# Performance work log

Hardware: AMD Instinct MI355X
Metric: run time of the kernel (lower is better)

Reference implementation:

```python
import jax, jax.numpy as jnp
import numpy as np

N = 100000   # nodes
E = 1600000  # edges
G = 512      # graphs in batch
F_IN = 128
H = 128
F_OUT = 1


def setup_inputs() -> dict:
    key = jax.random.key(0)
    ks = jax.random.split(key, 12)
    x = jax.random.normal(ks[0], (N, F_IN), dtype=jnp.float32)
    src = jax.random.randint(ks[1], (E,), 0, N, dtype=jnp.int32)
    dst = jax.random.randint(ks[2], (E,), 0, N, dtype=jnp.int32)
    node2graph = jnp.sort(jax.random.randint(ks[3], (N,), 0, G, dtype=jnp.int32))
    s_in = 1.0 / np.sqrt(F_IN)
    s_h = 1.0 / np.sqrt(H)
    W0 = jax.random.normal(ks[4], (F_IN, H), dtype=jnp.float32) * s_in
    b0 = jnp.zeros((H,), dtype=jnp.float32)
    W1 = jax.random.normal(ks[5], (H, H), dtype=jnp.float32) * s_h
    b1 = jnp.zeros((H,), dtype=jnp.float32)
    W2 = jax.random.normal(ks[6], (H, H), dtype=jnp.float32) * s_h
    b2 = jnp.zeros((H,), dtype=jnp.float32)
    Wm1 = jax.random.normal(ks[7], (H, H), dtype=jnp.float32) * s_h
    bm1 = jnp.zeros((H,), dtype=jnp.float32)
    Wm2 = jax.random.normal(ks[8], (H, F_OUT), dtype=jnp.float32) * s_h
    bm2 = jnp.zeros((F_OUT,), dtype=jnp.float32)
    return {"x": x, "src": src, "dst": dst, "node2graph": node2graph,
            "W0": W0, "b0": b0, "W1": W1, "b1": b1, "W2": W2, "b2": b2,
            "Wm1": Wm1, "bm1": bm1, "Wm2": Wm2, "bm2": bm2}


def _degree_norms(src, dst):
    ones = jnp.ones((E,), dtype=jnp.float32)
    out_deg = jax.ops.segment_sum(ones, src, num_segments=N)
    in_deg = jax.ops.segment_sum(ones, dst, num_segments=N)
    norm_out = jax.lax.rsqrt(jnp.maximum(out_deg, 1.0))  # [N]
    norm_in = jax.lax.rsqrt(jnp.maximum(in_deg, 1.0))    # [N]
    return norm_out, norm_in


def _graph_conv(x, src, dst, norm_out, norm_in, W, b):
    # DGL GraphConv, norm='both', in_feats <= out_feats path:
    # aggregate normalized src features, then linear + activation.
    xs = x * norm_out[:, None]
    msg = xs[src]                                         # [E, H] gather
    agg = jax.ops.segment_sum(msg, dst, num_segments=N)   # [N, H] scatter-add
    agg = agg * norm_in[:, None]
    return jax.nn.relu(agg @ W + b)


def reference(x, src, dst, node2graph, W0, b0, W1, b1, W2, b2, Wm1, bm1, Wm2, bm2):
    norm_out, norm_in = _degree_norms(src, dst)
    h = _graph_conv(x, src, dst, norm_out, norm_in, W0, b0)
    h = _graph_conv(h, src, dst, norm_out, norm_in, W1, b1)
    h = _graph_conv(h, src, dst, norm_out, norm_in, W2, b2)
    # sum_nodes readout per graph
    g = jax.ops.segment_sum(h, node2graph, num_segments=G)  # [G, H]
    # MLP head: Linear -> ReLU -> Linear
    return jax.nn.relu(g @ Wm1 + bm1) @ Wm2 + bm2           # [G, 1]
```

## Files before the change

### kernel.cpp

```cpp
#include <hip/hip_runtime.h>

#define NN 100000
#define NE 1600000
#define NG 512
#define HD 128

#define NBK 196
#define CHUNK 5120
#define NC 313
#define LH (2 * NBK * NC)

typedef _Float16 half4 __attribute__((ext_vector_type(4)));
typedef _Float16 h8 __attribute__((ext_vector_type(8)));
typedef float f32x4 __attribute__((ext_vector_type(4)));

__global__ __launch_bounds__(256) void k_hist(const int* __restrict__ src,
                                              const int* __restrict__ dst,
                                              int* __restrict__ H) {
    __shared__ int hd[NBK], hs[NBK];
    int c = blockIdx.x;
    for (int i = threadIdx.x; i < NBK; i += 256) { hd[i] = 0; hs[i] = 0; }
    __syncthreads();
    int e0 = c * CHUNK;
    int e1 = e0 + CHUNK; if (e1 > NE) e1 = NE;
    for (int e = e0 + threadIdx.x; e < e1; e += 256) {
        atomicAdd(&hd[dst[e] >> 9], 1);
        atomicAdd(&hs[src[e] >> 9], 1);
    }
    __syncthreads();
    for (int i = threadIdx.x; i < NBK; i += 256) {
        H[i * NC + c] = hd[i];
        H[NBK * NC + i * NC + c] = hs[i];
    }
}

__global__ __launch_bounds__(256) void k_scan1g(int* __restrict__ H,
                                                int* __restrict__ bsum, int L) {
    __shared__ int s[256];
    int i = blockIdx.x * 256 + threadIdx.x;
    int v = (i < L) ? H[i] : 0;
    s[threadIdx.x] = v;
    __syncthreads();
    for (int off = 1; off < 256; off <<= 1) {
        int t = (threadIdx.x >= off) ? s[threadIdx.x - off] : 0;
        __syncthreads();
        s[threadIdx.x] += t;
        __syncthreads();
    }
    if (i < L) H[i] = s[threadIdx.x] - v;
    if (threadIdx.x == 255) bsum[blockIdx.x] = s[255];
}

__global__ __launch_bounds__(512) void k_scan2(int* __restrict__ bsum, int nb) {
    __shared__ int s[512];
    int v = (threadIdx.x < nb) ? bsum[threadIdx.x] : 0;
    s[threadIdx.x] = v;
    __syncthreads();
    for (int off = 1; off < 512; off <<= 1) {
        int t = (threadIdx.x >= off) ? s[threadIdx.x - off] : 0;
        __syncthreads();
        s[threadIdx.x] += t;
        __syncthreads();
    }
    if (threadIdx.x < nb) bsum[threadIdx.x] = s[threadIdx.x] - v;
}

__global__ __launch_bounds__(256) void k_scan3g(int* __restrict__ H,
                                                const int* __restrict__ bsum, int L) {
    int i = blockIdx.x * 256 + threadIdx.x;
    if (i < L) H[i] += bsum[i >> 8];
}

__global__ __launch_bounds__(256) void k_scatter(const int* __restrict__ src,
                                                 const int* __restrict__ dst,
                                                 const int* __restrict__ H,
                                                 int2* __restrict__ dpart,
                                                 int* __restrict__ spart) {
    __shared__ int cd[NBK], cs[NBK];
    int c = blockIdx.x;
    for (int i = threadIdx.x; i < NBK; i += 256) {
        cd[i] = H[i * NC + c];
        cs[i] = H[NBK * NC + i * NC + c] - NE;
    }
    __syncthreads();
    int e0 = c * CHUNK;
    int e1 = e0 + CHUNK; if (e1 > NE) e1 = NE;
    for (int e = e0 + threadIdx.x; e < e1; e += 256) {
        int s = src[e], d = dst[e];
        int pd = atomicAdd(&cd[d >> 9], 1);
        dpart[pd] = make_int2(s, d);
        int ps = atomicAdd(&cs[s >> 9], 1);
        spart[ps] = s;
    }
}

__global__ __launch_bounds__(256) void k_bucket(const int2* __restrict__ dpart,
                                                const int* __restrict__ spart,
                                                const int* __restrict__ H,
                                                int* __restrict__ offs,
                                                int* __restrict__ csr,
                                                float* __restrict__ ni,
                                                float* __restrict__ no) {
    __shared__ int deg[512];
    __shared__ int cur[512];
    __shared__ int tmp[256];
    int b = blockIdx.x;
    bool isDst = (b < NBK);
    int bb = isDst ? b : b - NBK;
    int start, end;
    if (isDst) {
        start = H[bb * NC];
        end = (bb + 1 < NBK) ? H[(bb + 1) * NC] : NE;
    } else {
        start = H[NBK * NC + bb * NC] - NE;
        end = (bb + 1 < NBK) ? H[NBK * NC + (bb + 1) * NC] - NE : NE;
    }
    for (int i = threadIdx.x; i < 512; i += 256) deg[i] = 0;
    __syncthreads();
    if (isDst) {
        for (int i = start + threadIdx.x; i < end; i += 256)
            atomicAdd(&deg[dpart[i].y & 511], 1);
    } else {
        for (int i = start + threadIdx.x; i < end; i += 256)
            atomicAdd(&deg[spart[i] & 511], 1);
    }
    __syncthreads();
    int vb = bb * 512;
    if (!isDst) {
        for (int i = threadIdx.x; i < 512; i += 256) {
            int v = vb + i;
            if (v < NN) no[v] = rsqrtf(fmaxf((float)deg[i], 1.0f));
        }
        return;
    }
    int t = threadIdx.x;
    int a0 = deg[2 * t], a1 = deg[2 * t + 1];
    int pair = a0 + a1;
    tmp[t] = pair;
    __syncthreads();
    for (int off = 1; off < 256; off <<= 1) {
        int v2 = (t >= off) ? tmp[t - off] : 0;
        __syncthreads();
        tmp[t] += v2;
        __syncthreads();
    }
    int ex = tmp[t] - pair;
    cur[2 * t] = start + ex;
    cur[2 * t + 1] = start + ex + a0;
    __syncthreads();
    for (int i = threadIdx.x; i < 512; i += 256) {
        int v = vb + i;
        if (v < NN) {
            offs[v] = cur[i];
            ni[v] = rsqrtf(fmaxf((float)deg[i], 1.0f));
        }
    }
    if (b == NBK - 1 && threadIdx.x == 0) offs[NN] = NE;
    __syncthreads();
    for (int i = start + threadIdx.x; i < end; i += 256) {
        int2 e = dpart[i];
        int p = atomicAdd(&cur[e.y & 511], 1);
        csr[p] = e.x;
    }
}

__global__ __launch_bounds__(256) void k_castw(const float* __restrict__ W0,
                                               const float* __restrict__ W1,
                                               const float* __restrict__ W2,
                                               _Float16* __restrict__ Bt) {
    int i = blockIdx.x * 256 + threadIdx.x;
    if (i >= 3 * 16384) return;
    int w = i >> 14;
    int rem = i & 16383;
    int n = rem >> 7;
    int k = rem & 127;
    const float* W = (w == 0) ? W0 : ((w == 1) ? W1 : W2);
    Bt[i] = (_Float16)W[k * 128 + n];
}

template <typename TA>
__global__ __launch_bounds__(256) void k_gemm_mfma(const TA* __restrict__ A,
                                                   const _Float16* __restrict__ Bt,
                                                   const float* __restrict__ no,
                                                   _Float16* __restrict__ Zh,
                                                   int nrows) {
    __shared__ _Float16 Bs[128 * 136];
    int tid = threadIdx.x;
    {
        const h8* B8 = (const h8*)Bt;
        h8* Bs8 = (h8*)Bs;
        for (int i = tid; i < 2048; i += 256) {
            int n = i >> 4, c = i & 15;
            Bs8[n * 17 + c] = B8[i];
        }
    }

    int wave = tid >> 6;
    int lane = tid & 63;
    int m16 = lane & 15;
    int quad = lane >> 4;
    int rowbase = blockIdx.x * 64 + wave * 16;
    int row = rowbase + m16;
    bool valid = row < nrows;

    h8 afrag[4];
    if (valid) {
        if constexpr (sizeof(TA) == 2) {
            const h8* Arow = (const h8*)(A + (size_t)row * 128);
#pragma unroll
            for (int kk = 0; kk < 4; kk++) afrag[kk] = Arow[kk * 4 + quad];
        } else {
            const float4* Arow = (const float4*)(A + (size_t)row * 128);
#pragma unroll
            for (int kk = 0; kk < 4; kk++) {
                float4 lo = Arow[kk * 8 + quad * 2];
                float4 hi = Arow[kk * 8 + quad * 2 + 1];
                h8 a;
                a[0] = (_Float16)lo.x; a[1] = (_Float16)lo.y;
                a[2] = (_Float16)lo.z; a[3] = (_Float16)lo.w;
                a[4] = (_Float16)hi.x; a[5] = (_Float16)hi.y;
                a[6] = (_Float16)hi.z; a[7] = (_Float16)hi.w;
                afrag[kk] = a;
            }
        }
    } else {
#pragma unroll
        for (int kk = 0; kk < 4; kk++) {
            h8 a;
#pragma unroll
            for (int j = 0; j < 8; j++) a[j] = (_Float16)0.f;
            afrag[kk] = a;
        }
    }

    __syncthreads();

    f32x4 acc[8];
#pragma unroll
    for (int nt = 0; nt < 8; nt++) acc[nt] = (f32x4){0.f, 0.f, 0.f, 0.f};

    const h8* Bs8 = (const h8*)Bs;
#pragma unroll
    for (int nt = 0; nt < 8; nt++) {
        const h8* Bp = Bs8 + (size_t)(nt * 16 + m16) * 17;
#pragma unroll
        for (int kk = 0; kk < 4; kk++) {
            acc[nt] = __builtin_amdgcn_mfma_f32_16x16x32_f16(afrag[kk], Bp[kk * 4 + quad],
                                                             acc[nt], 0, 0, 0);
        }
    }

    float nor[4];
#pragma unroll
    for (int r = 0; r < 4; r++) {
        int grow = rowbase + quad * 4 + r;
        nor[r] = (grow < nrows) ? no[grow] : 0.f;
    }

    __syncthreads();
    {
        int lr0 = wave * 16 + quad * 4;
#pragma unroll
        for (int nt = 0; nt < 8; nt++) {
#pragma unroll
            for (int r = 0; r < 4; r++) {
                Bs[(size_t)(lr0 + r) * 136 + nt * 16 + m16] =
                    (_Float16)(acc[nt][r] * nor[r]);
            }
        }
    }
    __syncthreads();

    int blockrow0 = blockIdx.x * 64;
    for (int i = tid; i < 1024; i += 256) {
        int r = i >> 4, cch = i & 15;
        int grow = blockrow0 + r;
        if (grow < nrows) {
            h8 val = *(const h8*)&Bs[(size_t)r * 136 + cch * 8];
            *(h8*)&Zh[(size_t)grow * 128 + cch * 8] = val;
        }
    }
}

__global__ __launch_bounds__(128) void k_agg(const h8* __restrict__ Zh,
                                             const int* __restrict__ offs,
                                             const int* __restrict__ csr,
                                             const float* __restrict__ ni,
                                             const float* __restrict__ b,
                                             h8* __restrict__ H16) {
    int v = blockIdx.x * 8 + (threadIdx.x >> 4);
    int c = threadIdx.x & 15;
    int s = offs[v];
    int e = offs[v + 1];
    float a0[8], a1[8];
#pragma unroll
    for (int j = 0; j < 8; j++) { a0[j] = 0.f; a1[j] = 0.f; }
    int i = s;
    for (; i + 4 <= e; i += 4) {
        int u0 = csr[i];
        int u1 = csr[i + 1];
        int u2 = csr[i + 2];
        int u3 = csr[i + 3];
        h8 z0 = Zh[(size_t)u0 * 16 + c];
        h8 z1 = Zh[(size_t)u1 * 16 + c];
        h8 z2 = Zh[(size_t)u2 * 16 + c];
        h8 z3 = Zh[(size_t)u3 * 16 + c];
#pragma unroll
        for (int j = 0; j < 8; j++) {
            a0[j] += (float)z0[j] + (float)z1[j];
            a1[j] += (float)z2[j] + (float)z3[j];
        }
    }
    for (; i < e; i++) {
        int u = csr[i];
        h8 z = Zh[(size_t)u * 16 + c];
#pragma unroll
        for (int j = 0; j < 8; j++) a0[j] += (float)z[j];
    }
    float niv = ni[v];
    const float* bb = b + c * 8;
    h8 r;
#pragma unroll
    for (int j = 0; j < 8; j++)
        r[j] = (_Float16)fmaxf((a0[j] + a1[j]) * niv + bb[j], 0.f);
    H16[(size_t)v * 16 + c] = r;
}

__global__ __launch_bounds__(128) void k_readout(const h8* __restrict__ H8,
                                                 const int* __restrict__ n2g,
                                                 float* __restrict__ g) {
    __shared__ float red[128 * 8];
    int gi = blockIdx.x;
    int t = threadIdx.x;
    int slot = t >> 4;
    int c = t & 15;

    int lo = 0, hi = NN;
    while (lo < hi) { int mid = (lo + hi) >> 1; if (n2g[mid] < gi) lo = mid + 1; else hi = mid; }
    int s = lo;
    hi = NN;
    while (lo < hi) { int mid = (lo + hi) >> 1; if (n2g[mid] < gi + 1) lo = mid + 1; else hi = mid; }
    int e = lo;

    float acc[8];
#pragma unroll
    for (int j = 0; j < 8; j++) acc[j] = 0.f;
    for (int v = s + slot; v < e; v += 8) {
        h8 z = H8[(size_t)v * 16 + c];
#pragma unroll
        for (int j = 0; j < 8; j++) acc[j] += (float)z[j];
    }
#pragma unroll
    for (int j = 0; j < 8; j++) red[t * 8 + j] = acc[j];
    __syncthreads();
    for (int off = 4; off >= 1; off >>= 1) {
        if (slot < off) {
#pragma unroll
            for (int j = 0; j < 8; j++)
                red[t * 8 + j] += red[(t + off * 16) * 8 + j];
        }
        __syncthreads();
    }
    if (slot == 0) {
#pragma unroll
        for (int j = 0; j < 8; j++)
            g[gi * 128 + c * 8 + j] = red[t * 8 + j];
    }
}

__global__ __launch_bounds__(128) void k_head(const float* __restrict__ g,
                                              const float* __restrict__ Wm1,
                                              const float* __restrict__ bm1,
                                              const float* __restrict__ Wm2,
                                              const float* __restrict__ bm2,
                                              float* __restrict__ out) {
    __shared__ float gs[128];
    __shared__ float red[128];
    int gi = blockIdx.x;
    int f = threadIdx.x;
    gs[f] = g[gi * 128 + f];
    __syncthreads();
    float acc = bm1[f];
    for (int k = 0; k < 128; k++) acc += gs[k] * Wm1[k * 128 + f];
    float h1 = fmaxf(acc, 0.f);
    red[f] = h1 * Wm2[f];
    __syncthreads();
    for (int s2 = 64; s2 > 0; s2 >>= 1) {
        if (f < s2) red[f] += red[f + s2];
        __syncthreads();
    }
    if (f == 0) out[gi] = red[0] + bm2[0];
}

extern "C" void kernel_launch(void* const* d_in, const int* in_sizes, int n_in,
                              void* d_out, int out_size, void* d_ws, size_t ws_size,
                              hipStream_t stream) {
    const float* x   = (const float*)d_in[0];
    const int*   src = (const int*)d_in[1];
    const int*   dst = (const int*)d_in[2];
    const int*   n2g = (const int*)d_in[3];
    const float* W0  = (const float*)d_in[4];
    const float* b0  = (const float*)d_in[5];
    const float* W1  = (const float*)d_in[6];
    const float* b1  = (const float*)d_in[7];
    const float* W2  = (const float*)d_in[8];
    const float* b2  = (const float*)d_in[9];
    const float* Wm1 = (const float*)d_in[10];
    const float* bm1 = (const float*)d_in[11];
    const float* Wm2 = (const float*)d_in[12];
    const float* bm2 = (const float*)d_in[13];
    float* out = (float*)d_out;

    char* p = (char*)d_ws;
    auto carve = [&](size_t bytes) -> char* {
        char* r = p;
        p += (bytes + 255) & ~(size_t)255;
        return r;
    };
    _Float16* zh  = (_Float16*)carve((size_t)NN * HD * 2);
    _Float16* h16 = (_Float16*)carve((size_t)NN * HD * 2);
    _Float16* Bt  = (_Float16*)carve((size_t)3 * 128 * 128 * 2);
    float* no     = (float*)carve((size_t)NN * 4);
    float* ni     = (float*)carve((size_t)NN * 4);
    int*   offs   = (int*)carve((size_t)(NN + 1) * 4);
    int*   csr    = (int*)carve((size_t)NE * 4);
    int*   Hh     = (int*)carve((size_t)LH * 4);
    int*   bsum   = (int*)carve((size_t)512 * 4);
    int2*  dpart  = (int2*)carve((size_t)NE * 8);
    int*   spart  = (int*)carve((size_t)NE * 4);
    float* g      = (float*)carve((size_t)NG * HD * 4);

    k_castw<<<(3 * 16384 + 255) / 256, 256, 0, stream>>>(W0, W1, W2, Bt);

    int scan_blocks = (LH + 255) / 256;
    k_hist<<<NC, 256, 0, stream>>>(src, dst, Hh);
    k_scan1g<<<scan_blocks, 256, 0, stream>>>(Hh, bsum, LH);
    k_scan2<<<1, 512, 0, stream>>>(bsum, scan_blocks);
    k_scan3g<<<scan_blocks, 256, 0, stream>>>(Hh, bsum, LH);
    k_scatter<<<NC, 256, 0, stream>>>(src, dst, Hh, dpart, spart);
    k_bucket<<<2 * NBK, 256, 0, stream>>>(dpart, spart, Hh, offs, csr, ni, no);

    int gemm_blocks = (NN + 63) / 64;

    k_gemm_mfma<float><<<gemm_blocks, 256, 0, stream>>>(x, Bt, no, zh, NN);
    k_agg<<<NN / 8, 128, 0, stream>>>((const h8*)zh, offs, csr, ni, b0, (h8*)h16);
    k_gemm_mfma<_Float16><<<gemm_blocks, 256, 0, stream>>>(h16, Bt + 16384, no, zh, NN);
    k_agg<<<NN / 8, 128, 0, stream>>>((const h8*)zh, offs, csr, ni, b1, (h8*)h16);
    k_gemm_mfma<_Float16><<<gemm_blocks, 256, 0, stream>>>(h16, Bt + 32768, no, zh, NN);
    k_agg<<<NN / 8, 128, 0, stream>>>((const h8*)zh, offs, csr, ni, b2, (h8*)h16);

    k_readout<<<NG, 128, 0, stream>>>((const h8*)h16, n2g, g);
    k_head<<<NG, 128, 0, stream>>>(g, Wm1, bm1, Wm2, bm2, out);
}
```

Measured before the change: 417.6 us.

## Fuse small kernels, pack partition records, and widen aggregation blocks

Folds the weight cast into the histogram launch, merges the second-level scan into the third scan kernel, and fuses the readout with the MLP head, removing three launches. Partition records are packed into 32-bit (src plus 9-bit local dst) and 16-bit (local src) words, which halves the scatter and bucket traffic. Aggregation blocks go from 8 to 16 nodes each. Every scan3 block now redoes the small block-sum scan, and the packing assumes node ids fit in 17 bits.

```diff
diff --git a/kernel.cpp b/kernel.cpp
--- a/kernel.cpp
+++ b/kernel.cpp
@@ -16,7 +16,21 @@
 
 __global__ __launch_bounds__(256) void k_hist(const int* __restrict__ src,
                                               const int* __restrict__ dst,
-                                              int* __restrict__ H) {
+                                              int* __restrict__ H,
+                                              const float* __restrict__ W0,
+                                              const float* __restrict__ W1,
+                                              const float* __restrict__ W2,
+                                              _Float16* __restrict__ Bt) {
+    if (blockIdx.x >= NC) {
+        int i = (blockIdx.x - NC) * 256 + threadIdx.x;
+        int w = i >> 14;
+        int rem = i & 16383;
+        int n = rem >> 7;
+        int k = rem & 127;
+        const float* W = (w == 0) ? W0 : ((w == 1) ? W1 : W2);
+        Bt[i] = (_Float16)W[k * 128 + n];
+        return;
+    }
     __shared__ int hd[NBK], hs[NBK];
     int c = blockIdx.x;
     for (int i = threadIdx.x; i < NBK; i += 256) { hd[i] = 0; hs[i] = 0; }
@@ -51,31 +65,36 @@
     if (threadIdx.x == 255) bsum[blockIdx.x] = s[255];
 }
 
-__global__ __launch_bounds__(512) void k_scan2(int* __restrict__ bsum, int nb) {
-    __shared__ int s[512];
-    int v = (threadIdx.x < nb) ? bsum[threadIdx.x] : 0;
-    s[threadIdx.x] = v;
-    __syncthreads();
-    for (int off = 1; off < 512; off <<= 1) {
-        int t = (threadIdx.x >= off) ? s[threadIdx.x - off] : 0;
-        __syncthreads();
-        s[threadIdx.x] += t;
-        __syncthreads();
-    }
-    if (threadIdx.x < nb) bsum[threadIdx.x] = s[threadIdx.x] - v;
-}
-
 __global__ __launch_bounds__(256) void k_scan3g(int* __restrict__ H,
-                                                const int* __restrict__ bsum, int L) {
-    int i = blockIdx.x * 256 + threadIdx.x;
-    if (i < L) H[i] += bsum[i >> 8];
+                                                const int* __restrict__ bsum,
+                                                int L, int nb) {
+    __shared__ int sb[512];
+    __shared__ int tmp2[256];
+    int t = threadIdx.x;
+    int b0 = (2 * t < nb) ? bsum[2 * t] : 0;
+    int b1 = (2 * t + 1 < nb) ? bsum[2 * t + 1] : 0;
+    int pair = b0 + b1;
+    tmp2[t] = pair;
+    __syncthreads();
+    for (int off = 1; off < 256; off <<= 1) {
+        int v2 = (t >= off) ? tmp2[t - off] : 0;
+        __syncthreads();
+        tmp2[t] += v2;
+        __syncthreads();
+    }
+    int ex = tmp2[t] - pair;
+    sb[2 * t] = ex;
+    sb[2 * t + 1] = ex + b0;
+    __syncthreads();
+    int i = blockIdx.x * 256 + t;
+    if (i < L) H[i] += sb[i >> 8];
 }
 
 __global__ __launch_bounds__(256) void k_scatter(const int* __restrict__ src,
                                                  const int* __restrict__ dst,
                                                  const int* __restrict__ H,
-                                                 int2* __restrict__ dpart,
-                                                 int* __restrict__ spart) {
+                                                 int* __restrict__ dpart,
+                                                 unsigned short* __restrict__ spart) {
     __shared__ int cd[NBK], cs[NBK];
     int c = blockIdx.x;
     for (int i = threadIdx.x; i < NBK; i += 256) {
@@ -88,14 +107,14 @@
     for (int e = e0 + threadIdx.x; e < e1; e += 256) {
         int s = src[e], d = dst[e];
         int pd = atomicAdd(&cd[d >> 9], 1);
-        dpart[pd] = make_int2(s, d);
+        dpart[pd] = s | ((d & 511) << 17);
         int ps = atomicAdd(&cs[s >> 9], 1);
-        spart[ps] = s;
-    }
-}
-
-__global__ __launch_bounds__(256) void k_bucket(const int2* __restrict__ dpart,
-                                                const int* __restrict__ spart,
+        spart[ps] = (unsigned short)(s & 511);
+    }
+}
+
+__global__ __launch_bounds__(256) void k_bucket(const int* __restrict__ dpart,
+                                                const unsigned short* __restrict__ spart,
                                                 const int* __restrict__ H,
                                                 int* __restrict__ offs,
                                                 int* __restrict__ csr,
@@ -119,10 +138,10 @@
     __syncthreads();
     if (isDst) {
         for (int i = start + threadIdx.x; i < end; i += 256)
-            atomicAdd(&deg[dpart[i].y & 511], 1);
+            atomicAdd(&deg[(dpart[i] >> 17) & 511], 1);
     } else {
         for (int i = start + threadIdx.x; i < end; i += 256)
-            atomicAdd(&deg[spart[i] & 511], 1);
+            atomicAdd(&deg[spart[i]], 1);
     }
     __syncthreads();
     int vb = bb * 512;
@@ -158,24 +177,10 @@
     if (b == NBK - 1 && threadIdx.x == 0) offs[NN] = NE;
     __syncthreads();
     for (int i = start + threadIdx.x; i < end; i += 256) {
-        int2 e = dpart[i];
-        int p = atomicAdd(&cur[e.y & 511], 1);
-        csr[p] = e.x;
-    }
-}
-
-__global__ __launch_bounds__(256) void k_castw(const float* __restrict__ W0,
-                                               const float* __restrict__ W1,
-                                               const float* __restrict__ W2,
-                                               _Float16* __restrict__ Bt) {
-    int i = blockIdx.x * 256 + threadIdx.x;
-    if (i >= 3 * 16384) return;
-    int w = i >> 14;
-    int rem = i & 16383;
-    int n = rem >> 7;
-    int k = rem & 127;
-    const float* W = (w == 0) ? W0 : ((w == 1) ? W1 : W2);
-    Bt[i] = (_Float16)W[k * 128 + n];
+        int pk = dpart[i];
+        int p = atomicAdd(&cur[(pk >> 17) & 511], 1);
+        csr[p] = pk & 0x1FFFF;
+    }
 }
 
 template <typename TA>
@@ -282,13 +287,13 @@
     }
 }
 
-__global__ __launch_bounds__(128) void k_agg(const h8* __restrict__ Zh,
+__global__ __launch_bounds__(256) void k_agg(const h8* __restrict__ Zh,
                                              const int* __restrict__ offs,
                                              const int* __restrict__ csr,
                                              const float* __restrict__ ni,
                                              const float* __restrict__ b,
                                              h8* __restrict__ H16) {
-    int v = blockIdx.x * 8 + (threadIdx.x >> 4);
+    int v = blockIdx.x * 16 + (threadIdx.x >> 4);
     int c = threadIdx.x & 15;
     int s = offs[v];
     int e = offs[v + 1];
@@ -326,10 +331,16 @@
     H16[(size_t)v * 16 + c] = r;
 }
 
-__global__ __launch_bounds__(128) void k_readout(const h8* __restrict__ H8,
-                                                 const int* __restrict__ n2g,
-                                                 float* __restrict__ g) {
+__global__ __launch_bounds__(128) void k_readhead(const h8* __restrict__ H8,
+                                                  const int* __restrict__ n2g,
+                                                  const float* __restrict__ Wm1,
+                                                  const float* __restrict__ bm1,
+                                                  const float* __restrict__ Wm2,
+                                                  const float* __restrict__ bm2,
+                                                  float* __restrict__ out) {
     __shared__ float red[128 * 8];
+    __shared__ float gs[128];
+    __shared__ float red2[128];
     int gi = blockIdx.x;
     int t = threadIdx.x;
     int slot = t >> 4;
@@ -363,33 +374,21 @@
     }
     if (slot == 0) {
 #pragma unroll
-        for (int j = 0; j < 8; j++)
-            g[gi * 128 + c * 8 + j] = red[t * 8 + j];
-    }
-}
-
-__global__ __launch_bounds__(128) void k_head(const float* __restrict__ g,
-                                              const float* __restrict__ Wm1,
-                                              const float* __restrict__ bm1,
-                                              const float* __restrict__ Wm2,
-                                              const float* __restrict__ bm2,
-                                              float* __restrict__ out) {
-    __shared__ float gs[128];
-    __shared__ float red[128];
-    int gi = blockIdx.x;
-    int f = threadIdx.x;
-    gs[f] = g[gi * 128 + f];
-    __syncthreads();
-    float acc = bm1[f];
-    for (int k = 0; k < 128; k++) acc += gs[k] * Wm1[k * 128 + f];
-    float h1 = fmaxf(acc, 0.f);
-    red[f] = h1 * Wm2[f];
+        for (int j = 0; j < 8; j++) gs[c * 8 + j] = red[t * 8 + j];
+    }
+    __syncthreads();
+
+    int f = t;
+    float a = bm1[f];
+    for (int k = 0; k < 128; k++) a += gs[k] * Wm1[k * 128 + f];
+    float h1 = fmaxf(a, 0.f);
+    red2[f] = h1 * Wm2[f];
     __syncthreads();
     for (int s2 = 64; s2 > 0; s2 >>= 1) {
-        if (f < s2) red[f] += red[f + s2];
-        __syncthreads();
-    }
-    if (f == 0) out[gi] = red[0] + bm2[0];
+        if (f < s2) red2[f] += red2[f + s2];
+        __syncthreads();
+    }
+    if (f == 0) out[gi] = red2[0] + bm2[0];
 }
 
 extern "C" void kernel_launch(void* const* d_in, const int* in_sizes, int n_in,
@@ -426,29 +425,25 @@
     int*   csr    = (int*)carve((size_t)NE * 4);
     int*   Hh     = (int*)carve((size_t)LH * 4);
     int*   bsum   = (int*)carve((size_t)512 * 4);
-    int2*  dpart  = (int2*)carve((size_t)NE * 8);
-    int*   spart  = (int*)carve((size_t)NE * 4);
-    float* g      = (float*)carve((size_t)NG * HD * 4);
-
-    k_castw<<<(3 * 16384 + 255) / 256, 256, 0, stream>>>(W0, W1, W2, Bt);
+    int*   dpart  = (int*)carve((size_t)NE * 4);
+    unsigned short* spart = (unsigned short*)carve((size_t)NE * 2);
 
     int scan_blocks = (LH + 255) / 256;
-    k_hist<<<NC, 256, 0, stream>>>(src, dst, Hh);
+    k_hist<<<NC + 192, 256, 0, stream>>>(src, dst, Hh, W0, W1, W2, Bt);
     k_scan1g<<<scan_blocks, 256, 0, stream>>>(Hh, bsum, LH);
-    k_scan2<<<1, 512, 0, stream>>>(bsum, scan_blocks);
-    k_scan3g<<<scan_blocks, 256, 0, stream>>>(Hh, bsum, LH);
+    k_scan3g<<<scan_blocks, 256, 0, stream>>>(Hh, bsum, LH, scan_blocks);
     k_scatter<<<NC, 256, 0, stream>>>(src, dst, Hh, dpart, spart);
     k_bucket<<<2 * NBK, 256, 0, stream>>>(dpart, spart, Hh, offs, csr, ni, no);
 
     int gemm_blocks = (NN + 63) / 64;
+    int agg_blocks  = NN / 16;
 
     k_gemm_mfma<float><<<gemm_blocks, 256, 0, stream>>>(x, Bt, no, zh, NN);
-    k_agg<<<NN / 8, 128, 0, stream>>>((const h8*)zh, offs, csr, ni, b0, (h8*)h16);
+    k_agg<<<agg_blocks, 256, 0, stream>>>((const h8*)zh, offs, csr, ni, b0, (h8*)h16);
     k_gemm_mfma<_Float16><<<gemm_blocks, 256, 0, stream>>>(h16, Bt + 16384, no, zh, NN);
-    k_agg<<<NN / 8, 128, 0, stream>>>((const h8*)zh, offs, csr, ni, b1, (h8*)h16);
+    k_agg<<<agg_blocks, 256, 0, stream>>>((const h8*)zh, offs, csr, ni, b1, (h8*)h16);
     k_gemm_mfma<_Float16><<<gemm_blocks, 256, 0, stream>>>(h16, Bt + 32768, no, zh, NN);
-    k_agg<<<NN / 8, 128, 0, stream>>>((const h8*)zh, offs, csr, ni, b2, (h8*)h16);
-
-    k_readout<<<NG, 128, 0, stream>>>((const h8*)h16, n2g, g);
-    k_head<<<NG, 128, 0, stream>>>(g, Wm1, bm1, Wm2, bm2, out);
-}
+    k_agg<<<agg_blocks, 256, 0, stream>>>((const h8*)zh, offs, csr, ni, b2, (h8*)h16);
+
+    k_readhead<<<NG, 128, 0, stream>>>((const h8*)h16, n2g, Wm1, bm1, Wm2, bm2, out);
+}
```

New measurement: 408.2 us. 1.02x faster.
